# Kernel optimization log

Measured on AMD Instinct MI355X. Metric: run time of the kernel, lower is better.

Reference implementation:

```python
import jax, jax.numpy as jnp
import numpy as np

H = 16  # number of heads

def setup_inputs() -> dict:
    key = jax.random.key(0)
    ks = jax.random.split(key, 9)
    B, N, D = 2, 2048, 1024
    s = 0.02
    q = jax.random.normal(ks[0], (B, N, D), jnp.float32)
    k = jax.random.normal(ks[1], (B, N, D), jnp.float32)
    v = jax.random.normal(ks[2], (B, N, D), jnp.float32)
    mask = jax.random.randint(ks[3], (B, 1, N, N), 0, 2).astype(bool)
    Wq = jax.random.normal(ks[4], (D, D), jnp.float32) * s
    Wk = jax.random.normal(ks[5], (D, D), jnp.float32) * s
    Wv = jax.random.normal(ks[6], (D, D), jnp.float32) * s
    Wo = jax.random.normal(ks[7], (D, D), jnp.float32) * s
    bq = jnp.zeros((D,), jnp.float32)
    bk = jnp.zeros((D,), jnp.float32)
    bv = jnp.zeros((D,), jnp.float32)
    bo = jnp.zeros((D,), jnp.float32)
    return {"q": q, "k": k, "v": v, "mask": mask,
            "Wq": Wq, "bq": bq, "Wk": Wk, "bk": bk,
            "Wv": Wv, "bv": bv, "Wo": Wo, "bo": bo}


def reference(q, k, v, mask, Wq, bq, Wk, bk, Wv, bv, Wo, bo):
    B, N, D = q.shape
    dk = D // H
    # nn.Linear: x @ W.T + b, then split heads: b n (h d) -> b h n d
    def proj(x, W, b):
        return (x @ W.T + b).reshape(B, N, H, dk).transpose(0, 2, 1, 3)
    qh = proj(q, Wq, bq)  # [B,H,N,dk]
    kh = proj(k, Wk, bk)
    vh = proj(v, Wv, bv)
    # NOTE: original has NO 1/sqrt(dk) scaling
    score = jnp.einsum('bhnd,bhmd->bhnm', qh, kh)
    score = jnp.where(mask, jnp.float32(-1e9), score)
    attn = jax.nn.softmax(score, axis=-1)
    x = jnp.einsum('bhnm,bhmd->bhnd', attn, vh)
    x = x.transpose(0, 2, 1, 3).reshape(B, N, D)  # b h n d -> b n (h d)
    return x @ Wo.T + bo
```

## Files before the change

### kernel.cpp

```cpp
#include <hip/hip_runtime.h>
#include <math.h>

#define BB 2
#define NN 2048
#define DD 1024
#define HH 16
#define DK 64
#define LOG2E 1.4426950408889634f

typedef __attribute__((ext_vector_type(8))) short short8;
typedef __attribute__((ext_vector_type(4))) float f32x4;
typedef __attribute__((ext_vector_type(16))) float f32x16;
typedef __attribute__((ext_vector_type(4))) float f32x4v;
typedef __attribute__((ext_vector_type(8))) unsigned short ushort8;
typedef unsigned long long u64;

__device__ __forceinline__ unsigned short f2bf(float f) {
  unsigned u = __float_as_uint(f);
  unsigned r = (u + 0x7FFFu + ((u >> 16) & 1u)) >> 16;
  return (unsigned short)r;
}

__device__ __forceinline__ void gload_lds16(const void* g, void* l) {
  auto gp = (const __attribute__((address_space(1))) unsigned int*)(unsigned long long)g;
  auto lp = (__attribute__((address_space(3))) unsigned int*)(unsigned int)(unsigned long long)l;
  __builtin_amdgcn_global_load_lds(gp, lp, 16, 0, 0);
}

__global__ __launch_bounds__(256) void cvt_all(
    const float* __restrict__ q, const float* __restrict__ k, const float* __restrict__ v,
    const float* __restrict__ wq, const float* __restrict__ wk, const float* __restrict__ wv,
    const float* __restrict__ wo, unsigned short* __restrict__ ws)
{
  const long NW = (long)DD * DD;
  const long NX = (long)BB * NN * DD;
  long i = ((long)blockIdx.x * blockDim.x + threadIdx.x) * 8;
  if (i >= 4 * NW + 3 * NX) return;
  const float* src; unsigned short* dst; long off;
  if (i < 4 * NW) {
    int s = (int)(i / NW);
    src = (s == 0) ? wq : (s == 1) ? wk : (s == 2) ? wv : wo;
    off = i - (long)s * NW;
    dst = ws + (long)s * NW + off;
  } else {
    long j = i - 4 * NW;
    int s = (int)(j / NX);
    src = (s == 0) ? q : (s == 1) ? k : v;
    off = j - (long)s * NX;
    dst = ws + 4 * NW + (long)s * NX + off;
  }
  f32x4v a = *(const f32x4v*)(src + off);
  f32x4v b = *(const f32x4v*)(src + off + 4);
  ushort8 o;
  o[0] = f2bf(a[0]); o[1] = f2bf(a[1]); o[2] = f2bf(a[2]); o[3] = f2bf(a[3]);
  o[4] = f2bf(b[0]); o[5] = f2bf(b[1]); o[6] = f2bf(b[2]); o[7] = f2bf(b[3]);
  *(ushort8*)dst = o;
}

__global__ __launch_bounds__(256) void cvt_mask_bits(const void* __restrict__ mask,
                                                     u64* __restrict__ mb, long total64)
{
  const unsigned char* m8 = (const unsigned char*)mask;
  const int l = threadIdx.x & 63;
  unsigned probe = m8[l * 4 + 1] | m8[l * 4 + 2] | m8[l * 4 + 3];
  const bool isBool = (__any(probe != 0) != 0);

  long t = (long)blockIdx.x * blockDim.x + threadIdx.x;
  if (t >= total64) return;
  u64 bits = 0;
  if (isBool) {
    const uint4* p = (const uint4*)(m8 + t * 64);
#pragma unroll
    for (int i = 0; i < 4; ++i) {
      uint4 q4 = p[i];
      unsigned vv[4] = {q4.x, q4.y, q4.z, q4.w};
#pragma unroll
      for (int j = 0; j < 4; ++j)
#pragma unroll
        for (int bb = 0; bb < 4; ++bb)
          bits |= (u64)((vv[j] >> (8 * bb)) & 1u) << (i * 16 + j * 4 + bb);
    }
  } else {
    const int4* p = (const int4*)((const int*)mask + t * 64);
#pragma unroll
    for (int i = 0; i < 16; ++i) {
      int4 q4 = p[i];
      bits |= (u64)(q4.x & 1) << (i * 4);
      bits |= (u64)(q4.y & 1) << (i * 4 + 1);
      bits |= (u64)(q4.z & 1) << (i * 4 + 2);
      bits |= (u64)(q4.w & 1) << (i * 4 + 3);
    }
  }
  const long bb2 = t >> 16;
  const long qq = (t >> 5) & 2047;
  const long tcol = t & 31;
  mb[(bb2 * 32 + tcol) * 2048 + qq] = bits;
}

struct GemmArgs {
  const unsigned short* A;
  const unsigned short* Bw;
  const float* bias;
  void* C;
  int mode;
  float oscale;
};

__global__ __launch_bounds__(256) void gemm_bt(GemmArgs ga0, GemmArgs ga1, GemmArgs ga2)
{
  GemmArgs ga = (blockIdx.z == 0) ? ga0 : ((blockIdx.z == 1) ? ga1 : ga2);
  constexpr int K = DD;
  constexpr int Nn = DD;
  __shared__ __align__(16) unsigned short As[128 * 32];
  __shared__ __align__(16) unsigned short Bs[128 * 32];

  const int tid = threadIdx.x;
  const int lane = tid & 63;
  const int w = tid >> 6;
  const int wr = w >> 1, wc = w & 1;
  const int m0 = blockIdx.y * 128, n0 = blockIdx.x * 128;
  const int c = lane & 15, g = lane >> 4;

  f32x4 acc[4][4];
  const f32x4 z4 = {0.f, 0.f, 0.f, 0.f};
#pragma unroll
  for (int m = 0; m < 4; ++m)
#pragma unroll
    for (int n = 0; n < 4; ++n) acc[m][n] = z4;

  const unsigned short* Ab = ga.A + (long)m0 * K;
  const unsigned short* Bb = ga.Bw + (long)n0 * K;
  const int ar = tid >> 2;
  const int ac = (tid & 3) * 8;

  for (int kk = 0; kk < K; kk += 32) {
#pragma unroll
    for (int i = 0; i < 2; ++i) {
      gload_lds16(Ab + (long)(i * 64 + ar) * K + kk + ac, &As[i * 2048 + tid * 8]);
      gload_lds16(Bb + (long)(i * 64 + ar) * K + kk + ac, &Bs[i * 2048 + tid * 8]);
    }
    __syncthreads();

    short8 a[4], b[4];
#pragma unroll
    for (int m = 0; m < 4; ++m)
      a[m] = *(const short8*)&As[(wr * 64 + 16 * m + c) * 32 + g * 8];
#pragma unroll
    for (int n = 0; n < 4; ++n)
      b[n] = *(const short8*)&Bs[(wc * 64 + 16 * n + c) * 32 + g * 8];
#pragma unroll
    for (int m = 0; m < 4; ++m)
#pragma unroll
      for (int n = 0; n < 4; ++n)
        acc[m][n] = __builtin_amdgcn_mfma_f32_16x16x32_bf16(a[m], b[n], acc[m][n], 0, 0, 0);
    __syncthreads();
  }

#pragma unroll
  for (int n = 0; n < 4; ++n) {
    const int col = n0 + wc * 64 + 16 * n + c;
    const float bv = ga.bias[col];
#pragma unroll
    for (int m = 0; m < 4; ++m) {
      const int row0 = m0 + wr * 64 + 16 * m + 4 * g;
#pragma unroll
      for (int r = 0; r < 4; ++r) {
        const int row = row0 + r;
        const float val = (acc[m][n][r] + bv) * ga.oscale;
        if (ga.mode == 1)
          ((float*)ga.C)[(long)row * Nn + col] = val;
        else if (ga.mode == 0)
          ((unsigned short*)ga.C)[(long)row * Nn + col] = f2bf(val);
        else
          ((unsigned short*)ga.C)[((long)(row >> 11) * DD + col) * NN + (row & (NN - 1))] = f2bf(val);
      }
    }
  }
}

__global__ __launch_bounds__(256, 2) void attn_kernel(
    const unsigned short* __restrict__ Q,
    const unsigned short* __restrict__ K,
    const unsigned short* __restrict__ Vt,
    const u64* __restrict__ mb64,
    unsigned short* __restrict__ ctx)
{
  __shared__ __align__(16) unsigned short Ks[2][64 * 64];
  __shared__ __align__(16) unsigned short Vs[2][64 * 64];

  const int tid = threadIdx.x;
  const int lane = tid & 63;
  const int w = tid >> 6;
  const int bid = blockIdx.x;
  const int b = (bid >> 4) & 1, h = bid & 15;
  const int q0 = (bid >> 5) * 128;
  const int l31 = lane & 31;
  const int hi = lane >> 5;
  const int qrow = q0 + 32 * w + l31;

  short8 aq[4];
  {
    const unsigned short* qp = Q + ((long)(b * NN + qrow)) * DD + h * DK + 8 * hi;
    aq[0] = *(const short8*)(qp);
    aq[1] = *(const short8*)(qp + 16);
    aq[2] = *(const short8*)(qp + 32);
    aq[3] = *(const short8*)(qp + 48);
  }

  f32x16 o0, o1, cinit;
#pragma unroll
  for (int r = 0; r < 16; ++r) { o0[r] = 0.f; o1[r] = 0.f; cinit[r] = -28.853901f; }
  float lsum = 0.f;

  const unsigned short* Kbase = K + (long)(b * NN) * DD + h * DK;
  const unsigned short* Vbase = Vt + ((long)(b * DD + h * DK)) * NN;
  const u64* mbase = mb64 + (long)(b * 32) * 2048 + qrow;

  const int srow = tid >> 3;
  const int scol = tid & 7;
  const int swcol = scol ^ (srow & 7);

  auto STAGE = [&](int buf, int t) {
#pragma unroll
    for (int hf = 0; hf < 2; ++hf) {
      const int row = srow + 32 * hf;
      gload_lds16(Kbase + (long)(t * 64 + row) * DD + swcol * 8, &Ks[buf][hf * 2048 + tid * 8]);
      gload_lds16(Vbase + (long)row * NN + t * 64 + swcol * 8, &Vs[buf][hf * 2048 + tid * 8]);
    }
  };

  STAGE(0, 0);
  __syncthreads();
  int cur = 0;
  const int sh4 = 4 * hi;

  for (int t = 0; t < 32; ++t) {
    if (t < 31) STAGE(cur ^ 1, t + 1);
    const u64 mword = mbase[(long)t * 2048];
    const unsigned msk0 = ((unsigned)mword) >> sh4;
    const unsigned msk1 = ((unsigned)(mword >> 32)) >> sh4;

#pragma unroll
    for (int sub = 0; sub < 2; ++sub) {
      const unsigned m = sub ? msk1 : msk0;
      const int krow = l31 + 32 * sub;
      const int kswz = (krow & 7) << 3;

      f32x16 ss = cinit;
#pragma unroll
      for (int i = 0; i < 4; ++i) {
        const short8 kf = *(const short8*)&Ks[cur][krow * 64 + ((16 * i + 8 * hi) ^ kswz)];
        ss = __builtin_amdgcn_mfma_f32_32x32x16_bf16(kf, aq[i], ss, 0, 0, 0);
      }

      float p[16];
#pragma unroll
      for (int r = 0; r < 16; ++r) {
        const int cr = (r & 3) + 8 * (r >> 2);
        const float e = ((m >> cr) & 1u) ? -1e9f : ss[r];
        p[r] = __builtin_amdgcn_exp2f(e);
        lsum += p[r];
      }

      unsigned wv[8];
#pragma unroll
      for (int i = 0; i < 8; ++i) {
        unsigned rr;
        asm("v_cvt_pk_bf16_f32 %0, %1, %2" : "=v"(rr) : "v"(p[2 * i]), "v"(p[2 * i + 1]));
        wv[i] = rr;
      }
      asm("v_permlane32_swap_b32 %0, %1" : "+v"(wv[0]), "+v"(wv[2]));
      asm("v_permlane32_swap_b32 %0, %1" : "+v"(wv[1]), "+v"(wv[3]));
      asm("v_permlane32_swap_b32 %0, %1" : "+v"(wv[4]), "+v"(wv[6]));
      asm("v_permlane32_swap_b32 %0, %1" : "+v"(wv[5]), "+v"(wv[7]));
      union { short8 s; unsigned u[4]; } pa0, pa1;
      pa0.u[0] = wv[0]; pa0.u[1] = wv[1]; pa0.u[2] = wv[2]; pa0.u[3] = wv[3];
      pa1.u[0] = wv[4]; pa1.u[1] = wv[5]; pa1.u[2] = wv[6]; pa1.u[3] = wv[7];

#pragma unroll
      for (int dblk = 0; dblk < 2; ++dblk) {
        const int vrow = l31 + 32 * dblk;
        const int vswz = (vrow & 7) << 3;
        const short8 vb0 = *(const short8*)&Vs[cur][vrow * 64 + ((32 * sub + 8 * hi) ^ vswz)];
        const short8 vb1 = *(const short8*)&Vs[cur][vrow * 64 + ((32 * sub + 16 + 8 * hi) ^ vswz)];
        if (dblk == 0) {
          o0 = __builtin_amdgcn_mfma_f32_32x32x16_bf16(pa0.s, vb0, o0, 0, 0, 0);
          o0 = __builtin_amdgcn_mfma_f32_32x32x16_bf16(pa1.s, vb1, o0, 0, 0, 0);
        } else {
          o1 = __builtin_amdgcn_mfma_f32_32x32x16_bf16(pa0.s, vb0, o1, 0, 0, 0);
          o1 = __builtin_amdgcn_mfma_f32_32x32x16_bf16(pa1.s, vb1, o1, 0, 0, 0);
        }
      }
    }
    __syncthreads();
    cur ^= 1;
  }

  lsum += __shfl_xor(lsum, 32);
  const float inv = 1.0f / lsum;

#pragma unroll
  for (int r = 0; r < 16; ++r) {
    const int qr = (r & 3) + 8 * (r >> 2) + 4 * hi;
    const float linv = __shfl(inv, qr);
    const long row = (long)(b * NN + q0 + 32 * w + qr);
    ctx[row * DD + h * DK + l31] = f2bf(o0[r] * linv);
    ctx[row * DD + h * DK + 32 + l31] = f2bf(o1[r] * linv);
  }
}

extern "C" void kernel_launch(void* const* d_in, const int* in_sizes, int n_in,
                              void* d_out, int out_size, void* d_ws, size_t ws_size,
                              hipStream_t stream) {
  const float* q  = (const float*)d_in[0];
  const float* k  = (const float*)d_in[1];
  const float* v  = (const float*)d_in[2];
  const void*  mask = d_in[3];
  const float* Wq = (const float*)d_in[4];
  const float* bq = (const float*)d_in[5];
  const float* Wk = (const float*)d_in[6];
  const float* bk = (const float*)d_in[7];
  const float* Wv = (const float*)d_in[8];
  const float* bv = (const float*)d_in[9];
  const float* Wo = (const float*)d_in[10];
  const float* bo = (const float*)d_in[11];

  unsigned short* ws = (unsigned short*)d_ws;
  const long NW = (long)DD * DD;
  const long NX = (long)BB * NN * DD;
  unsigned short* Wqb = ws;
  unsigned short* Wkb = ws + NW;
  unsigned short* Wvb = ws + 2 * NW;
  unsigned short* Wob = ws + 3 * NW;
  unsigned short* Xq  = ws + 4 * NW;
  unsigned short* Xk  = Xq + NX;
  unsigned short* Xv  = Xk + NX;
  unsigned short* Qh  = Xv + NX;
  unsigned short* Kh  = Qh + NX;
  unsigned short* Vtr = Kh + NX;
  unsigned short* Ctx = Vtr + NX;
  u64* Mbits = (u64*)(Ctx + NX);
  const long NM64 = (long)BB * NN * NN / 64;

  cvt_all<<<8192, 256, 0, stream>>>(q, k, v, Wq, Wk, Wv, Wo, ws);
  cvt_mask_bits<<<(int)(NM64 / 256), 256, 0, stream>>>(mask, Mbits, NM64);

  GemmArgs gq = {Xq, Wqb, bq, (void*)Qh, 0, LOG2E};
  GemmArgs gk = {Xk, Wkb, bk, (void*)Kh, 0, 1.0f};
  GemmArgs gv = {Xv, Wvb, bv, (void*)Vtr, 2, 1.0f};
  dim3 gproj(DD / 128, (BB * NN) / 128, 3);
  gemm_bt<<<gproj, 256, 0, stream>>>(gq, gk, gv);

  attn_kernel<<<512, 256, 0, stream>>>(Qh, Kh, Vtr, Mbits, Ctx);

  GemmArgs go = {Ctx, Wob, bo, d_out, 1, 1.0f};
  dim3 gout(DD / 128, (BB * NN) / 128, 1);
  gemm_bt<<<gout, 256, 0, stream>>>(go, go, go);
}
```

Baseline: 150.4 us.

## Remap GEMM workgroups across XCDs, use 64-row tiles for output GEMM, prefetch mask, setprio

The GEMM kernel is templated on tile height. Workgroup IDs are remapped so consecutive tiles land on the same XCD chiplet, which should improve L2 reuse. The output projection uses 64x128 tiles, doubling its block count so more CUs are busy for the small single-GEMM launch. In attention, the next mask word is loaded one iteration ahead, and the MFMA sections are wrapped in s_setprio so matrix work gets scheduling priority over the softmax ALU work of other waves.

```diff
diff --git a/kernel.cpp b/kernel.cpp
--- a/kernel.cpp
+++ b/kernel.cpp
@@ -106,27 +106,40 @@
   float oscale;
 };
 
+template<int TM>
 __global__ __launch_bounds__(256) void gemm_bt(GemmArgs ga0, GemmArgs ga1, GemmArgs ga2)
 {
-  GemmArgs ga = (blockIdx.z == 0) ? ga0 : ((blockIdx.z == 1) ? ga1 : ga2);
   constexpr int K = DD;
   constexpr int Nn = DD;
-  __shared__ __align__(16) unsigned short As[128 * 32];
+  constexpr int PERZ_LOG = (TM == 128) ? 8 : 9;
+  constexpr int NF = (TM == 128) ? 4 : 2;
+  __shared__ __align__(16) unsigned short As[TM * 32];
   __shared__ __align__(16) unsigned short Bs[128 * 32];
+
+  const int gy = (TM == 128) ? 32 : 64;
+  int wgid = blockIdx.x + ((blockIdx.y + blockIdx.z * gy) << 3);
+  const int nwg = (int)gridDim.z << PERZ_LOG;
+  const int chunk = nwg >> 3;
+  wgid = (wgid & 7) * chunk + (wgid >> 3);
+  const int zi = wgid >> PERZ_LOG;
+  const int rem = wgid & ((1 << PERZ_LOG) - 1);
+  const int m0 = (rem >> 3) * TM;
+  const int n0 = (rem & 7) * 128;
+  GemmArgs ga = (zi == 0) ? ga0 : ((zi == 1) ? ga1 : ga2);
 
   const int tid = threadIdx.x;
   const int lane = tid & 63;
   const int w = tid >> 6;
-  const int wr = w >> 1, wc = w & 1;
-  const int m0 = blockIdx.y * 128, n0 = blockIdx.x * 128;
+  const int m_woff = (TM == 128) ? (w >> 1) * 64 : 0;
+  const int n_woff = (TM == 128) ? (w & 1) * 64 : w * 32;
   const int c = lane & 15, g = lane >> 4;
 
-  f32x4 acc[4][4];
+  f32x4 acc[4][NF];
   const f32x4 z4 = {0.f, 0.f, 0.f, 0.f};
 #pragma unroll
   for (int m = 0; m < 4; ++m)
 #pragma unroll
-    for (int n = 0; n < 4; ++n) acc[m][n] = z4;
+    for (int n = 0; n < NF; ++n) acc[m][n] = z4;
 
   const unsigned short* Ab = ga.A + (long)m0 * K;
   const unsigned short* Bb = ga.Bw + (long)n0 * K;
@@ -135,34 +148,35 @@
 
   for (int kk = 0; kk < K; kk += 32) {
 #pragma unroll
-    for (int i = 0; i < 2; ++i) {
+    for (int i = 0; i < TM / 64; ++i)
       gload_lds16(Ab + (long)(i * 64 + ar) * K + kk + ac, &As[i * 2048 + tid * 8]);
+#pragma unroll
+    for (int i = 0; i < 2; ++i)
       gload_lds16(Bb + (long)(i * 64 + ar) * K + kk + ac, &Bs[i * 2048 + tid * 8]);
-    }
     __syncthreads();
 
-    short8 a[4], b[4];
+    short8 a[4], b[NF];
 #pragma unroll
     for (int m = 0; m < 4; ++m)
-      a[m] = *(const short8*)&As[(wr * 64 + 16 * m + c) * 32 + g * 8];
-#pragma unroll
-    for (int n = 0; n < 4; ++n)
-      b[n] = *(const short8*)&Bs[(wc * 64 + 16 * n + c) * 32 + g * 8];
+      a[m] = *(const short8*)&As[(m_woff + 16 * m + c) * 32 + g * 8];
+#pragma unroll
+    for (int n = 0; n < NF; ++n)
+      b[n] = *(const short8*)&Bs[(n_woff + 16 * n + c) * 32 + g * 8];
 #pragma unroll
     for (int m = 0; m < 4; ++m)
 #pragma unroll
-      for (int n = 0; n < 4; ++n)
+      for (int n = 0; n < NF; ++n)
         acc[m][n] = __builtin_amdgcn_mfma_f32_16x16x32_bf16(a[m], b[n], acc[m][n], 0, 0, 0);
     __syncthreads();
   }
 
 #pragma unroll
-  for (int n = 0; n < 4; ++n) {
-    const int col = n0 + wc * 64 + 16 * n + c;
+  for (int n = 0; n < NF; ++n) {
+    const int col = n0 + n_woff + 16 * n + c;
     const float bv = ga.bias[col];
 #pragma unroll
     for (int m = 0; m < 4; ++m) {
-      const int row0 = m0 + wr * 64 + 16 * m + 4 * g;
+      const int row0 = m0 + m_woff + 16 * m + 4 * g;
 #pragma unroll
       for (int r = 0; r < 4; ++r) {
         const int row = row0 + r;
@@ -233,10 +247,11 @@
   __syncthreads();
   int cur = 0;
   const int sh4 = 4 * hi;
+  u64 mword = mbase[0];
 
   for (int t = 0; t < 32; ++t) {
+    const u64 mnext = (t < 31) ? mbase[(long)(t + 1) * 2048] : 0;
     if (t < 31) STAGE(cur ^ 1, t + 1);
-    const u64 mword = mbase[(long)t * 2048];
     const unsigned msk0 = ((unsigned)mword) >> sh4;
     const unsigned msk1 = ((unsigned)(mword >> 32)) >> sh4;
 
@@ -247,11 +262,13 @@
       const int kswz = (krow & 7) << 3;
 
       f32x16 ss = cinit;
+      __builtin_amdgcn_s_setprio(1);
 #pragma unroll
       for (int i = 0; i < 4; ++i) {
         const short8 kf = *(const short8*)&Ks[cur][krow * 64 + ((16 * i + 8 * hi) ^ kswz)];
         ss = __builtin_amdgcn_mfma_f32_32x32x16_bf16(kf, aq[i], ss, 0, 0, 0);
       }
+      __builtin_amdgcn_s_setprio(0);
 
       float p[16];
 #pragma unroll
@@ -277,6 +294,7 @@
       pa0.u[0] = wv[0]; pa0.u[1] = wv[1]; pa0.u[2] = wv[2]; pa0.u[3] = wv[3];
       pa1.u[0] = wv[4]; pa1.u[1] = wv[5]; pa1.u[2] = wv[6]; pa1.u[3] = wv[7];
 
+      __builtin_amdgcn_s_setprio(1);
 #pragma unroll
       for (int dblk = 0; dblk < 2; ++dblk) {
         const int vrow = l31 + 32 * dblk;
@@ -291,9 +309,11 @@
           o1 = __builtin_amdgcn_mfma_f32_32x32x16_bf16(pa1.s, vb1, o1, 0, 0, 0);
         }
       }
+      __builtin_amdgcn_s_setprio(0);
     }
     __syncthreads();
     cur ^= 1;
+    mword = mnext;
   }
 
   lsum += __shfl_xor(lsum, 32);
@@ -349,11 +369,11 @@
   GemmArgs gk = {Xk, Wkb, bk, (void*)Kh, 0, 1.0f};
   GemmArgs gv = {Xv, Wvb, bv, (void*)Vtr, 2, 1.0f};
   dim3 gproj(DD / 128, (BB * NN) / 128, 3);
-  gemm_bt<<<gproj, 256, 0, stream>>>(gq, gk, gv);
+  gemm_bt<128><<<gproj, 256, 0, stream>>>(gq, gk, gv);
 
   attn_kernel<<<512, 256, 0, stream>>>(Qh, Kh, Vtr, Mbits, Ctx);
 
   GemmArgs go = {Ctx, Wob, bo, d_out, 1, 1.0f};
-  dim3 gout(DD / 128, (BB * NN) / 128, 1);
-  gemm_bt<<<gout, 256, 0, stream>>>(go, go, go);
-}
+  dim3 gout(DD / 128, (BB * NN) / 64, 1);
+  gemm_bt<64><<<gout, 256, 0, stream>>>(go, go, go);
+}
```

New measurement: 146.6 us. 1.03x faster.
